# Kernel optimization log

Hardware: AMD Instinct MI355X
Metric: run time of the kernel (lower is better)

The kernel has to match this reference:

```python
import jax, jax.numpy as jnp
import numpy as np

N = 50000        # nodes
E = 800000       # edges (avg degree 16)
F_IN = 128       # input feature dim == heads*hidden of every layer
H = 4            # heads per layer
C = 32           # hidden (per-head out) per layer
ED = 16          # edge_dim
L = 3            # num GAT layers
NEG_SLOPE = 0.2  # PyG GATConv default


def setup_inputs() -> dict:
    key = jax.random.key(0)
    ks = jax.random.split(key, 13)
    s = 0.1
    x = jax.random.normal(ks[0], (N, F_IN), jnp.float32)
    edge_index = jax.random.randint(ks[1], (2, E), 0, N, dtype=jnp.int32)
    edge_attr = jax.random.normal(ks[2], (E, ED), jnp.float32)
    # stacked per-layer GATConv params (all layers are 128 -> 4x32)
    W_src = jax.random.normal(ks[3], (L, F_IN, H * C), jnp.float32) * s
    att_src = jax.random.normal(ks[4], (L, H, C), jnp.float32) * s
    att_dst = jax.random.normal(ks[5], (L, H, C), jnp.float32) * s
    W_edge = jax.random.normal(ks[6], (L, ED, H * C), jnp.float32) * s
    att_edge = jax.random.normal(ks[7], (L, H, C), jnp.float32) * s
    bias = jnp.zeros((L, H * C), jnp.float32)
    # dense head: Linear(128,256) -> ReLU -> Linear(256,2)
    W1 = jax.random.normal(ks[8], (H * C, 2 * H * C), jnp.float32) * s
    b1 = jnp.zeros((2 * H * C,), jnp.float32)
    W2 = jax.random.normal(ks[9], (2 * H * C, 2), jnp.float32) * s
    b2 = jnp.zeros((2,), jnp.float32)
    return {"x": x, "edge_index": edge_index, "edge_attr": edge_attr,
            "W_src": W_src, "att_src": att_src, "att_dst": att_dst,
            "W_edge": W_edge, "att_edge": att_edge, "bias": bias,
            "W1": W1, "b1": b1, "W2": W2, "b2": b2}


def reference(x, edge_index, edge_attr, W_src, att_src, att_dst,
              W_edge, att_edge, bias, W1, b1, W2, b2):
    src, dst = edge_index[0], edge_index[1]
    # add_self_loops with fill_value='mean': self-loop edge_attr = mean of
    # incoming edge attrs per node (0 if no incoming edges)
    deg = jax.ops.segment_sum(jnp.ones((E,), x.dtype), dst, num_segments=N)
    loop_attr = jax.ops.segment_sum(edge_attr, dst, num_segments=N) \
        / jnp.maximum(deg, 1.0)[:, None]
    nodes = jnp.arange(N, dtype=src.dtype)
    src_f = jnp.concatenate([src, nodes])          # [E+N]
    dst_f = jnp.concatenate([dst, nodes])          # [E+N]
    ea = jnp.concatenate([edge_attr, loop_attr], axis=0)  # [E+N, ED]

    h = x
    for l in range(L):
        hp = (h @ W_src[l]).reshape(N, H, C)                 # [N,H,C]
        a_s = (hp * att_src[l]).sum(-1)                      # [N,H]
        a_d = (hp * att_dst[l]).sum(-1)                      # [N,H]
        ef = (ea @ W_edge[l]).reshape(-1, H, C)              # [E+N,H,C]
        a_e = (ef * att_edge[l]).sum(-1)                     # [E+N,H]
        alpha = jax.nn.leaky_relu(a_s[src_f] + a_d[dst_f] + a_e, NEG_SLOPE)
        # segment softmax over destination node (self-loops ensure coverage)
        m = jax.ops.segment_max(alpha, dst_f, num_segments=N)
        ex = jnp.exp(alpha - m[dst_f])
        denom = jax.ops.segment_sum(ex, dst_f, num_segments=N)
        w = ex / denom[dst_f]                                # [E+N,H]
        agg = jax.ops.segment_sum(w[:, :, None] * hp[src_f], dst_f,
                                  num_segments=N)            # [N,H,C]
        h = jax.nn.relu(agg.reshape(N, H * C) + bias[l])

    g = h.mean(axis=0, keepdims=True)                        # batch=None -> [1,128]
    hid = jax.nn.relu(g @ W1 + b1)
    return hid @ W2 + b2                                     # [1,2]
```

## Files before the change

kernel.cpp:

```cpp
#include <hip/hip_runtime.h>
#include <math.h>

#define N_NODES 50000
#define N_EDGES 800000
#define F 128
#define H 4
#define C 32
#define ED 16
#define L 3
#define NEG 0.2f
#define ET (N_EDGES + N_NODES)
#define SCAN_B ((N_NODES + 255) / 256)
#define POOL_B 1024

typedef unsigned short bf16_t;

__device__ __forceinline__ bf16_t f2bf(float f) {
    unsigned u = __float_as_uint(f);
    unsigned r = (u + 0x7fffu + ((u >> 16) & 1u)) >> 16;
    return (bf16_t)r;
}
__device__ __forceinline__ float bf2f(bf16_t b) {
    return __uint_as_float(((unsigned)b) << 16);
}


__global__ void k_count(const int* __restrict__ dst, int* __restrict__ deg) {
    int e = blockIdx.x * 256 + threadIdx.x;
    if (e < N_EDGES) atomicAdd(&deg[dst[e]], 1);
}

__global__ __launch_bounds__(256) void k_scanA(const int* __restrict__ deg,
                                               int* __restrict__ off, int* __restrict__ bsum) {
    __shared__ int sh[256];
    int t = threadIdx.x;
    int i = blockIdx.x * 256 + t;
    int v = (i < N_NODES) ? (deg[i] + 1) : 0;
    sh[t] = v;
    __syncthreads();
    #pragma unroll
    for (int d = 1; d < 256; d <<= 1) {
        int u = (t >= d) ? sh[t - d] : 0;
        __syncthreads();
        sh[t] += u;
        __syncthreads();
    }
    if (i < N_NODES) off[i] = sh[t] - v;
    if (t == 255) bsum[blockIdx.x] = sh[255];
}

__global__ __launch_bounds__(256) void k_scanB(const int* __restrict__ bsum,
                                               int* __restrict__ boff, int* __restrict__ off) {
    __shared__ int sh[256];
    int t = threadIdx.x;
    int v = (t < SCAN_B) ? bsum[t] : 0;
    sh[t] = v;
    __syncthreads();
    #pragma unroll
    for (int d = 1; d < 256; d <<= 1) {
        int u = (t >= d) ? sh[t - d] : 0;
        __syncthreads();
        sh[t] += u;
        __syncthreads();
    }
    if (t < SCAN_B) boff[t] = sh[t] - v;
    if (t == 255) off[N_NODES] = sh[255];
}

__global__ void k_scanC(int* __restrict__ off, const int* __restrict__ boff) {
    int i = blockIdx.x * 256 + threadIdx.x;
    if (i < N_NODES) off[i] += boff[blockIdx.x];
}

__global__ void k_scatter(const int* __restrict__ ei, const int* __restrict__ off,
                          int* __restrict__ cursor, int* __restrict__ src_csr,
                          int* __restrict__ eid_csr) {
    int e = blockIdx.x * 256 + threadIdx.x;
    if (e < N_EDGES) {
        int d = ei[N_EDGES + e];
        int p = atomicAdd(&cursor[d], 1);
        int slot = off[d] + p;
        src_csr[slot] = ei[e];
        eid_csr[slot] = e;
    } else if (e < ET) {
        int nn = e - N_EDGES;
        int p = atomicAdd(&cursor[nn], 1);
        int slot = off[nn] + p;
        src_csr[slot] = nn;
        eid_csr[slot] = e;
    }
}

__global__ void k_we2(const float* __restrict__ W_edge, const float* __restrict__ att_edge,
                      float* __restrict__ we2) {
    int idx = blockIdx.x * 64 + threadIdx.x;
    if (idx >= L * ED * H) return;
    int l = idx / (ED * H);
    int r = idx % (ED * H);
    int d = r / H, h = r % H;
    float s = 0.f;
    for (int c = 0; c < C; c++)
        s += W_edge[(size_t)(l * ED + d) * (H * C) + h * C + c] * att_edge[(l * H + h) * C + c];
    we2[idx] = s;
}


#define BM 64
#define BK 32
__global__ __launch_bounds__(256) void k_gemm(const float* __restrict__ A,
                                              const float* __restrict__ W,
                                              const float* __restrict__ att_src_l,
                                              const float* __restrict__ att_dst_l,
                                              bf16_t* __restrict__ hpb,
                                              float* __restrict__ a_s,
                                              float* __restrict__ a_d) {
    __shared__ float As[BM][BK + 1];
    __shared__ float Bs[BK][F];
    int block_row = blockIdx.x * BM;
    int t = threadIdx.x;
    int tx = t & 31;
    int ty = t >> 5;
    float acc[8][4] = {};
    for (int k0 = 0; k0 < F; k0 += BK) {
        #pragma unroll
        for (int i = 0; i < 2; i++) {
            int idx = t + i * 256;
            int r = idx >> 3, cq = idx & 7;
            int gr = block_row + r;
            float4 v = make_float4(0.f, 0.f, 0.f, 0.f);
            if (gr < N_NODES) v = *(const float4*)&A[(size_t)gr * F + k0 + cq * 4];
            As[r][cq * 4 + 0] = v.x; As[r][cq * 4 + 1] = v.y;
            As[r][cq * 4 + 2] = v.z; As[r][cq * 4 + 3] = v.w;
        }
        #pragma unroll
        for (int i = 0; i < 4; i++) {
            int idx = t + i * 256;
            int r = idx >> 5, cq = idx & 31;
            float4 v = *(const float4*)&W[(size_t)(k0 + r) * F + cq * 4];
            *(float4*)&Bs[r][cq * 4] = v;
        }
        __syncthreads();
        for (int kk = 0; kk < BK; kk++) {
            float b[4];
            #pragma unroll
            for (int j = 0; j < 4; j++) b[j] = Bs[kk][tx + 32 * j];
            #pragma unroll
            for (int i = 0; i < 8; i++) {
                float a = As[ty * 8 + i][kk];
                #pragma unroll
                for (int j = 0; j < 4; j++) acc[i][j] += a * b[j];
            }
        }
        __syncthreads();
    }
    float avs[4], avd[4];
    #pragma unroll
    for (int j = 0; j < 4; j++) {
        avs[j] = att_src_l[j * 32 + tx];
        avd[j] = att_dst_l[j * 32 + tx];
    }
    #pragma unroll
    for (int i = 0; i < 8; i++) {
        int gr = block_row + ty * 8 + i;
        bool ok = (gr < N_NODES);
        if (ok) {
            #pragma unroll
            for (int j = 0; j < 4; j++) hpb[(size_t)gr * F + tx + 32 * j] = f2bf(acc[i][j]);
        }
        #pragma unroll
        for (int j = 0; j < 4; j++) {
            float vs = acc[i][j] * avs[j];
            float vd = acc[i][j] * avd[j];
            #pragma unroll
            for (int m = 1; m < 32; m <<= 1) {
                vs += __shfl_xor(vs, m, 64);
                vd += __shfl_xor(vd, m, 64);
            }
            if (tx == 0 && ok) {
                a_s[gr * H + j] = vs;
                a_d[gr * H + j] = vd;
            }
        }
    }
}

__global__ __launch_bounds__(256) void k_alpha(const int* __restrict__ eid_csr,
                                               const int* __restrict__ src_csr,
                                               const int* __restrict__ off,
                                               const float* __restrict__ edge_attr,
                                               const float* __restrict__ we2l,
                                               const float* __restrict__ a_s,
                                               const float* __restrict__ a_d,
                                               float* __restrict__ alpha_csr) {
    int n = blockIdx.x * 4 + (threadIdx.x >> 6);
    if (n >= N_NODES) return;
    int lane = threadIdx.x & 63;
    int beg = off[n], end = off[n + 1];
    float4 w[ED];
    #pragma unroll
    for (int k = 0; k < ED; k++) w[k] = *(const float4*)&we2l[k * 4];
    float4 adn = *(const float4*)&a_d[(size_t)n * 4];
    float sx = 0.f, sy = 0.f, sz = 0.f, sw = 0.f;
    int self_slot = -1;
    for (int i = beg + lane; i < end; i += 64) {
        int eid = eid_csr[i];
        if (eid < N_EDGES) {
            int src = src_csr[i];
            float4 asrc = *(const float4*)&a_s[(size_t)src * 4];
            const float* ea = &edge_attr[(size_t)eid * ED];
            float eav[ED];
            #pragma unroll
            for (int q = 0; q < ED / 4; q++) {
                float4 v = *(const float4*)&ea[q * 4];
                eav[q * 4 + 0] = v.x; eav[q * 4 + 1] = v.y;
                eav[q * 4 + 2] = v.z; eav[q * 4 + 3] = v.w;
            }
            float ax = 0.f, ay = 0.f, az = 0.f, aw = 0.f;
            #pragma unroll
            for (int k = 0; k < ED; k++) {
                float v = eav[k];
                ax += v * w[k].x; ay += v * w[k].y;
                az += v * w[k].z; aw += v * w[k].w;
            }
            sx += ax; sy += ay; sz += az; sw += aw;
            float4 o;
            o.x = asrc.x + adn.x + ax; o.x = (o.x > 0.f) ? o.x : NEG * o.x;
            o.y = asrc.y + adn.y + ay; o.y = (o.y > 0.f) ? o.y : NEG * o.y;
            o.z = asrc.z + adn.z + az; o.z = (o.z > 0.f) ? o.z : NEG * o.z;
            o.w = asrc.w + adn.w + aw; o.w = (o.w > 0.f) ? o.w : NEG * o.w;
            *(float4*)&alpha_csr[(size_t)i * H] = o;
        } else {
            self_slot = i;
        }
    }
    #pragma unroll
    for (int m = 1; m < 64; m <<= 1) {
        sx += __shfl_xor(sx, m, 64);
        sy += __shfl_xor(sy, m, 64);
        sz += __shfl_xor(sz, m, 64);
        sw += __shfl_xor(sw, m, 64);
    }
    if (self_slot >= 0) {
        float inv = 1.f / fmaxf((float)(end - beg - 1), 1.f);
        float4 asn = *(const float4*)&a_s[(size_t)n * 4];
        float4 o;
        o.x = asn.x + adn.x + sx * inv; o.x = (o.x > 0.f) ? o.x : NEG * o.x;
        o.y = asn.y + adn.y + sy * inv; o.y = (o.y > 0.f) ? o.y : NEG * o.y;
        o.z = asn.z + adn.z + sz * inv; o.z = (o.z > 0.f) ? o.z : NEG * o.z;
        o.w = asn.w + adn.w + sw * inv; o.w = (o.w > 0.f) ? o.w : NEG * o.w;
        *(float4*)&alpha_csr[(size_t)self_slot * H] = o;
    }
}

__global__ __launch_bounds__(256) void k_agg(const int* __restrict__ src_csr, const int* __restrict__ off,
                                             const float* __restrict__ alpha_csr,
                                             const bf16_t* __restrict__ hpb, const float* __restrict__ bias_l,
                                             float* __restrict__ hout) {
    int n = blockIdx.x * 4 + (threadIdx.x >> 6);
    if (n >= N_NODES) return;
    int lane = threadIdx.x & 63;
    int h = lane >> 4;
    int beg = off[n], end = off[n + 1];
    float accA0 = 0.f, accA1 = 0.f, accA2 = 0.f, accA3 = 0.f;
    float accB0 = 0.f, accB1 = 0.f, accB2 = 0.f, accB3 = 0.f;
    float den0 = 0.f, den1 = 0.f, den2 = 0.f, den3 = 0.f;
    int i = beg;
    for (; i + 4 <= end; i += 4) {
        int s0 = src_csr[i], s1 = src_csr[i + 1], s2 = src_csr[i + 2], s3 = src_csr[i + 3];
        float a0 = alpha_csr[(size_t)i * H + h];
        float a1 = alpha_csr[(size_t)(i + 1) * H + h];
        float a2 = alpha_csr[(size_t)(i + 2) * H + h];
        float a3 = alpha_csr[(size_t)(i + 3) * H + h];
        ushort2 v0 = *(const ushort2*)&hpb[(size_t)s0 * F + 2 * lane];
        ushort2 v1 = *(const ushort2*)&hpb[(size_t)s1 * F + 2 * lane];
        ushort2 v2 = *(const ushort2*)&hpb[(size_t)s2 * F + 2 * lane];
        ushort2 v3 = *(const ushort2*)&hpb[(size_t)s3 * F + 2 * lane];
        float e0 = __expf(a0), e1 = __expf(a1), e2 = __expf(a2), e3 = __expf(a3);
        accA0 += e0 * bf2f(v0.x); accB0 += e0 * bf2f(v0.y);
        accA1 += e1 * bf2f(v1.x); accB1 += e1 * bf2f(v1.y);
        accA2 += e2 * bf2f(v2.x); accB2 += e2 * bf2f(v2.y);
        accA3 += e3 * bf2f(v3.x); accB3 += e3 * bf2f(v3.y);
        den0 += e0; den1 += e1; den2 += e2; den3 += e3;
    }
    for (; i < end; i++) {
        int s0 = src_csr[i];
        float a0 = alpha_csr[(size_t)i * H + h];
        ushort2 v0 = *(const ushort2*)&hpb[(size_t)s0 * F + 2 * lane];
        float e0 = __expf(a0);
        accA0 += e0 * bf2f(v0.x); accB0 += e0 * bf2f(v0.y);
        den0 += e0;
    }
    float accA = (accA0 + accA1) + (accA2 + accA3);
    float accB = (accB0 + accB1) + (accB2 + accB3);
    float den  = (den0 + den1) + (den2 + den3);
    float2 bia = *(const float2*)&bias_l[2 * lane];
    float2 o;
    o.x = fmaxf(accA / den + bia.x, 0.f);
    o.y = fmaxf(accB / den + bia.y, 0.f);
    *(float2*)&hout[(size_t)n * F + 2 * lane] = o;
}


__global__ __launch_bounds__(256) void k_poolA(const float* __restrict__ hfinal,
                                               float* __restrict__ partials) {
    int t = threadIdx.x;
    int c = t & 127;
    int half = t >> 7;
    int b = blockIdx.x;
    float s = 0.f;
    for (int n = b * 2 + half; n < N_NODES; n += 2 * POOL_B)
        s += hfinal[(size_t)n * F + c];
    partials[(size_t)c * (2 * POOL_B) + b * 2 + half] = s;
}

__global__ __launch_bounds__(256) void k_poolB(const float* __restrict__ partials,
                                               float* __restrict__ gsum) {
    __shared__ float red[256];
    int c = blockIdx.x;
    int t = threadIdx.x;
    const float* row = &partials[(size_t)c * (2 * POOL_B)];
    float s = 0.f;
    for (int k = t; k < 2 * POOL_B; k += 256) s += row[k];
    red[t] = s;
    __syncthreads();
    for (int stp = 128; stp > 0; stp >>= 1) {
        if (t < stp) red[t] += red[t + stp];
        __syncthreads();
    }
    if (t == 0) gsum[c] = red[0];
}

__global__ __launch_bounds__(256) void k_mlp(const float* __restrict__ gsum, const float* __restrict__ W1,
                                             const float* __restrict__ b1, const float* __restrict__ W2,
                                             const float* __restrict__ b2, float* __restrict__ out) {
    __shared__ float g[F];
    __shared__ float hid[2 * F];
    __shared__ float red[256];
    int t = threadIdx.x;
    if (t < F) g[t] = gsum[t] * (1.0f / N_NODES);
    __syncthreads();
    float s = b1[t];
    for (int k = 0; k < F; k++) s += g[k] * W1[k * (2 * F) + t];
    hid[t] = fmaxf(s, 0.f);
    __syncthreads();
    for (int i = 0; i < 2; i++) {
        red[t] = hid[t] * W2[t * 2 + i];
        __syncthreads();
        for (int stp = 128; stp > 0; stp >>= 1) {
            if (t < stp) red[t] += red[t + stp];
            __syncthreads();
        }
        if (t == 0) out[i] = red[0] + b2[i];
        __syncthreads();
    }
}


extern "C" void kernel_launch(void* const* d_in, const int* in_sizes, int n_in,
                              void* d_out, int out_size, void* d_ws, size_t ws_size,
                              hipStream_t stream) {
    const float* x        = (const float*)d_in[0];
    const int*   ei       = (const int*)d_in[1];
    const float* edge_attr= (const float*)d_in[2];
    const float* W_src    = (const float*)d_in[3];
    const float* att_src  = (const float*)d_in[4];
    const float* att_dst  = (const float*)d_in[5];
    const float* W_edge   = (const float*)d_in[6];
    const float* att_edge = (const float*)d_in[7];
    const float* bias     = (const float*)d_in[8];
    const float* W1       = (const float*)d_in[9];
    const float* b1       = (const float*)d_in[10];
    const float* W2       = (const float*)d_in[11];
    const float* b2       = (const float*)d_in[12];
    float* out = (float*)d_out;

    char* p = (char*)d_ws;
    auto alloc = [&](size_t bytes) -> char* {
        char* r = p;
        p += (bytes + 255) & ~(size_t)255;
        return r;
    };
    int*      deg      = (int*)alloc((size_t)N_NODES * 4);
    int*      cursor   = (int*)alloc((size_t)N_NODES * 4);
    int*      off      = (int*)alloc((size_t)(N_NODES + 1) * 4);
    int*      bsum     = (int*)alloc((size_t)SCAN_B * 4);
    int*      boff     = (int*)alloc((size_t)SCAN_B * 4);
    int*      src_csr  = (int*)alloc((size_t)ET * 4);
    int*      eid_csr  = (int*)alloc((size_t)ET * 4);
    float*    we2      = (float*)alloc((size_t)L * ED * H * 4);
    float*    a_s      = (float*)alloc((size_t)N_NODES * H * 4);
    float*    a_d      = (float*)alloc((size_t)N_NODES * H * 4);
    float*    alpha_csr= (float*)alloc((size_t)ET * H * 4);
    bf16_t*   hpb      = (bf16_t*)alloc((size_t)N_NODES * F * 2);
    float*    hA       = (float*)alloc((size_t)N_NODES * F * 4);
    float*    hB       = (float*)alloc((size_t)N_NODES * F * 4);
    float*    partials = (float*)alloc((size_t)F * 2 * POOL_B * 4);
    float*    gsum     = (float*)alloc((size_t)F * 4);

    hipMemsetAsync(deg, 0, (size_t)N_NODES * 4, stream);
    hipMemsetAsync(cursor, 0, (size_t)N_NODES * 4, stream);

    const int* dst = ei + N_EDGES;
    k_count<<<(N_EDGES + 255) / 256, 256, 0, stream>>>(dst, deg);
    k_scanA<<<SCAN_B, 256, 0, stream>>>(deg, off, bsum);
    k_scanB<<<1, 256, 0, stream>>>(bsum, boff, off);
    k_scanC<<<SCAN_B, 256, 0, stream>>>(off, boff);
    k_scatter<<<(ET + 255) / 256, 256, 0, stream>>>(ei, off, cursor, src_csr, eid_csr);
    k_we2<<<3, 64, 0, stream>>>(W_edge, att_edge, we2);

    const float* hin = x;
    float* houts[3] = {hA, hB, hA};
    for (int l = 0; l < L; l++) {
        k_gemm<<<(N_NODES + BM - 1) / BM, 256, 0, stream>>>(hin, W_src + (size_t)l * F * F,
                                                            att_src + l * H * C, att_dst + l * H * C,
                                                            hpb, a_s, a_d);
        k_alpha<<<(N_NODES + 3) / 4, 256, 0, stream>>>(eid_csr, src_csr, off, edge_attr,
                                                       we2 + l * ED * H, a_s, a_d, alpha_csr);
        k_agg<<<(N_NODES + 3) / 4, 256, 0, stream>>>(src_csr, off, alpha_csr, hpb,
                                                     bias + l * F, houts[l]);
        hin = houts[l];
    }
    k_poolA<<<POOL_B, 256, 0, stream>>>(hA, partials);
    k_poolB<<<F, 256, 0, stream>>>(partials, gsum);
    k_mlp<<<1, 256, 0, stream>>>(gsum, W1, b1, W2, b2, out);
}
```

Before: 571.4 us.

## Fuse edge attention scoring into aggregation kernel and pack CSR src/eid pairs

```diff
diff --git a/kernel.cpp b/kernel.cpp
--- a/kernel.cpp
+++ b/kernel.cpp
@@ -73,21 +73,16 @@
 }
 
 __global__ void k_scatter(const int* __restrict__ ei, const int* __restrict__ off,
-                          int* __restrict__ cursor, int* __restrict__ src_csr,
-                          int* __restrict__ eid_csr) {
+                          int* __restrict__ cursor, int2* __restrict__ se_csr) {
     int e = blockIdx.x * 256 + threadIdx.x;
     if (e < N_EDGES) {
         int d = ei[N_EDGES + e];
         int p = atomicAdd(&cursor[d], 1);
-        int slot = off[d] + p;
-        src_csr[slot] = ei[e];
-        eid_csr[slot] = e;
+        se_csr[off[d] + p] = make_int2(ei[e], e);
     } else if (e < ET) {
         int nn = e - N_EDGES;
         int p = atomicAdd(&cursor[nn], 1);
-        int slot = off[nn] + p;
-        src_csr[slot] = nn;
-        eid_csr[slot] = e;
+        se_csr[off[nn] + p] = make_int2(nn, e);
     }
 }
 
@@ -184,115 +179,50 @@
     }
 }
 
-__global__ __launch_bounds__(256) void k_alpha(const int* __restrict__ eid_csr,
-                                               const int* __restrict__ src_csr,
-                                               const int* __restrict__ off,
-                                               const float* __restrict__ edge_attr,
-                                               const float* __restrict__ we2l,
-                                               const float* __restrict__ a_s,
-                                               const float* __restrict__ a_d,
-                                               float* __restrict__ alpha_csr) {
+__global__ __launch_bounds__(256) void k_fagg(const int2* __restrict__ se_csr,
+                                              const int* __restrict__ off,
+                                              const float* __restrict__ edge_attr,
+                                              const float* __restrict__ we2l,
+                                              const float* __restrict__ a_s,
+                                              const float* __restrict__ a_d,
+                                              const bf16_t* __restrict__ hpb,
+                                              const float* __restrict__ bias_l,
+                                              float* __restrict__ hout) {
     int n = blockIdx.x * 4 + (threadIdx.x >> 6);
     if (n >= N_NODES) return;
     int lane = threadIdx.x & 63;
+    int k = lane & 15, h = lane >> 4;
+    float myw = we2l[k * H + h];
     int beg = off[n], end = off[n + 1];
-    float4 w[ED];
-    #pragma unroll
-    for (int k = 0; k < ED; k++) w[k] = *(const float4*)&we2l[k * 4];
-    float4 adn = *(const float4*)&a_d[(size_t)n * 4];
-    float sx = 0.f, sy = 0.f, sz = 0.f, sw = 0.f;
-    int self_slot = -1;
-    for (int i = beg + lane; i < end; i += 64) {
-        int eid = eid_csr[i];
-        if (eid < N_EDGES) {
-            int src = src_csr[i];
-            float4 asrc = *(const float4*)&a_s[(size_t)src * 4];
-            const float* ea = &edge_attr[(size_t)eid * ED];
-            float eav[ED];
-            #pragma unroll
-            for (int q = 0; q < ED / 4; q++) {
-                float4 v = *(const float4*)&ea[q * 4];
-                eav[q * 4 + 0] = v.x; eav[q * 4 + 1] = v.y;
-                eav[q * 4 + 2] = v.z; eav[q * 4 + 3] = v.w;
-            }
-            float ax = 0.f, ay = 0.f, az = 0.f, aw = 0.f;
-            #pragma unroll
-            for (int k = 0; k < ED; k++) {
-                float v = eav[k];
-                ax += v * w[k].x; ay += v * w[k].y;
-                az += v * w[k].z; aw += v * w[k].w;
-            }
-            sx += ax; sy += ay; sz += az; sw += aw;
-            float4 o;
-            o.x = asrc.x + adn.x + ax; o.x = (o.x > 0.f) ? o.x : NEG * o.x;
-            o.y = asrc.y + adn.y + ay; o.y = (o.y > 0.f) ? o.y : NEG * o.y;
-            o.z = asrc.z + adn.z + az; o.z = (o.z > 0.f) ? o.z : NEG * o.z;
-            o.w = asrc.w + adn.w + aw; o.w = (o.w > 0.f) ? o.w : NEG * o.w;
-            *(float4*)&alpha_csr[(size_t)i * H] = o;
-        } else {
-            self_slot = i;
-        }
-    }
-    #pragma unroll
-    for (int m = 1; m < 64; m <<= 1) {
-        sx += __shfl_xor(sx, m, 64);
-        sy += __shfl_xor(sy, m, 64);
-        sz += __shfl_xor(sz, m, 64);
-        sw += __shfl_xor(sw, m, 64);
-    }
-    if (self_slot >= 0) {
-        float inv = 1.f / fmaxf((float)(end - beg - 1), 1.f);
-        float4 asn = *(const float4*)&a_s[(size_t)n * 4];
-        float4 o;
-        o.x = asn.x + adn.x + sx * inv; o.x = (o.x > 0.f) ? o.x : NEG * o.x;
-        o.y = asn.y + adn.y + sy * inv; o.y = (o.y > 0.f) ? o.y : NEG * o.y;
-        o.z = asn.z + adn.z + sz * inv; o.z = (o.z > 0.f) ? o.z : NEG * o.z;
-        o.w = asn.w + adn.w + sw * inv; o.w = (o.w > 0.f) ? o.w : NEG * o.w;
-        *(float4*)&alpha_csr[(size_t)self_slot * H] = o;
-    }
-}
-
-__global__ __launch_bounds__(256) void k_agg(const int* __restrict__ src_csr, const int* __restrict__ off,
-                                             const float* __restrict__ alpha_csr,
-                                             const bf16_t* __restrict__ hpb, const float* __restrict__ bias_l,
-                                             float* __restrict__ hout) {
-    int n = blockIdx.x * 4 + (threadIdx.x >> 6);
-    if (n >= N_NODES) return;
-    int lane = threadIdx.x & 63;
-    int h = lane >> 4;
-    int beg = off[n], end = off[n + 1];
-    float accA0 = 0.f, accA1 = 0.f, accA2 = 0.f, accA3 = 0.f;
-    float accB0 = 0.f, accB1 = 0.f, accB2 = 0.f, accB3 = 0.f;
-    float den0 = 0.f, den1 = 0.f, den2 = 0.f, den3 = 0.f;
-    int i = beg;
-    for (; i + 4 <= end; i += 4) {
-        int s0 = src_csr[i], s1 = src_csr[i + 1], s2 = src_csr[i + 2], s3 = src_csr[i + 3];
-        float a0 = alpha_csr[(size_t)i * H + h];
-        float a1 = alpha_csr[(size_t)(i + 1) * H + h];
-        float a2 = alpha_csr[(size_t)(i + 2) * H + h];
-        float a3 = alpha_csr[(size_t)(i + 3) * H + h];
-        ushort2 v0 = *(const ushort2*)&hpb[(size_t)s0 * F + 2 * lane];
-        ushort2 v1 = *(const ushort2*)&hpb[(size_t)s1 * F + 2 * lane];
-        ushort2 v2 = *(const ushort2*)&hpb[(size_t)s2 * F + 2 * lane];
-        ushort2 v3 = *(const ushort2*)&hpb[(size_t)s3 * F + 2 * lane];
-        float e0 = __expf(a0), e1 = __expf(a1), e2 = __expf(a2), e3 = __expf(a3);
-        accA0 += e0 * bf2f(v0.x); accB0 += e0 * bf2f(v0.y);
-        accA1 += e1 * bf2f(v1.x); accB1 += e1 * bf2f(v1.y);
-        accA2 += e2 * bf2f(v2.x); accB2 += e2 * bf2f(v2.y);
-        accA3 += e3 * bf2f(v3.x); accB3 += e3 * bf2f(v3.y);
-        den0 += e0; den1 += e1; den2 += e2; den3 += e3;
-    }
-    for (; i < end; i++) {
-        int s0 = src_csr[i];
-        float a0 = alpha_csr[(size_t)i * H + h];
-        ushort2 v0 = *(const ushort2*)&hpb[(size_t)s0 * F + 2 * lane];
-        float e0 = __expf(a0);
-        accA0 += e0 * bf2f(v0.x); accB0 += e0 * bf2f(v0.y);
-        den0 += e0;
-    }
-    float accA = (accA0 + accA1) + (accA2 + accA3);
-    float accB = (accB0 + accB1) + (accB2 + accB3);
-    float den  = (den0 + den1) + (den2 + den3);
+    float adn = a_d[(size_t)n * H + h];
+    float accA = 0.f, accB = 0.f, den = 0.f, sae = 0.f;
+    for (int i = beg; i < end; i++) {
+        int2 se = se_csr[i];
+        if (se.y < N_EDGES) {
+            float v = edge_attr[(size_t)se.y * ED + k];
+            float p = v * myw;
+            p += __shfl_xor(p, 1, 64);
+            p += __shfl_xor(p, 2, 64);
+            p += __shfl_xor(p, 4, 64);
+            p += __shfl_xor(p, 8, 64);
+            sae += p;
+            float al = a_s[(size_t)se.x * H + h] + adn + p;
+            al = (al > 0.f) ? al : NEG * al;
+            float e = __expf(al);
+            ushort2 v2 = *(const ushort2*)&hpb[(size_t)se.x * F + 2 * lane];
+            accA += e * bf2f(v2.x);
+            accB += e * bf2f(v2.y);
+            den += e;
+        }
+    }
+    float inv = 1.f / fmaxf((float)(end - beg - 1), 1.f);
+    float al = a_s[(size_t)n * H + h] + adn + sae * inv;
+    al = (al > 0.f) ? al : NEG * al;
+    float e = __expf(al);
+    ushort2 v2 = *(const ushort2*)&hpb[(size_t)n * F + 2 * lane];
+    accA += e * bf2f(v2.x);
+    accB += e * bf2f(v2.y);
+    den += e;
     float2 bia = *(const float2*)&bias_l[2 * lane];
     float2 o;
     o.x = fmaxf(accA / den + bia.x, 0.f);
@@ -385,12 +315,10 @@
     int*      off      = (int*)alloc((size_t)(N_NODES + 1) * 4);
     int*      bsum     = (int*)alloc((size_t)SCAN_B * 4);
     int*      boff     = (int*)alloc((size_t)SCAN_B * 4);
-    int*      src_csr  = (int*)alloc((size_t)ET * 4);
-    int*      eid_csr  = (int*)alloc((size_t)ET * 4);
+    int2*     se_csr   = (int2*)alloc((size_t)ET * 8);
     float*    we2      = (float*)alloc((size_t)L * ED * H * 4);
     float*    a_s      = (float*)alloc((size_t)N_NODES * H * 4);
     float*    a_d      = (float*)alloc((size_t)N_NODES * H * 4);
-    float*    alpha_csr= (float*)alloc((size_t)ET * H * 4);
     bf16_t*   hpb      = (bf16_t*)alloc((size_t)N_NODES * F * 2);
     float*    hA       = (float*)alloc((size_t)N_NODES * F * 4);
     float*    hB       = (float*)alloc((size_t)N_NODES * F * 4);
@@ -405,7 +333,7 @@
     k_scanA<<<SCAN_B, 256, 0, stream>>>(deg, off, bsum);
     k_scanB<<<1, 256, 0, stream>>>(bsum, boff, off);
     k_scanC<<<SCAN_B, 256, 0, stream>>>(off, boff);
-    k_scatter<<<(ET + 255) / 256, 256, 0, stream>>>(ei, off, cursor, src_csr, eid_csr);
+    k_scatter<<<(ET + 255) / 256, 256, 0, stream>>>(ei, off, cursor, se_csr);
     k_we2<<<3, 64, 0, stream>>>(W_edge, att_edge, we2);
 
     const float* hin = x;
@@ -414,10 +342,9 @@
         k_gemm<<<(N_NODES + BM - 1) / BM, 256, 0, stream>>>(hin, W_src + (size_t)l * F * F,
                                                             att_src + l * H * C, att_dst + l * H * C,
                                                             hpb, a_s, a_d);
-        k_alpha<<<(N_NODES + 3) / 4, 256, 0, stream>>>(eid_csr, src_csr, off, edge_attr,
-                                                       we2 + l * ED * H, a_s, a_d, alpha_csr);
-        k_agg<<<(N_NODES + 3) / 4, 256, 0, stream>>>(src_csr, off, alpha_csr, hpb,
-                                                     bias + l * F, houts[l]);
+        k_fagg<<<(N_NODES + 3) / 4, 256, 0, stream>>>(se_csr, off, edge_attr,
+                                                      we2 + l * ED * H, a_s, a_d,
+                                                      hpb, bias + l * F, houts[l]);
         hin = houts[l];
     }
     k_poolA<<<POOL_B, 256, 0, stream>>>(hA, partials);
```

New measurement: 765.5 us. +34.0%, slower.
